# Optimization experiments

Hardware: AMD Instinct MI355X
Metric: run time of the kernel (lower is better)

Reference implementation:

```python
import jax, jax.numpy as jnp
import numpy as np

N_NODES = 100000
N_EDGES = 1600000
IN_FEATS = 128
HEADS = 4
OUT_FEATS = 32
NEG_SLOPE = 0.2


def setup_inputs() -> dict:
    key = jax.random.key(0)
    ks = jax.random.split(key, 7)
    x = jax.random.normal(ks[0], (N_NODES, IN_FEATS), dtype=jnp.float32)
    fc_w = jax.random.normal(ks[1], (HEADS * OUT_FEATS, IN_FEATS), dtype=jnp.float32) * (1.0 / np.sqrt(IN_FEATS))
    attn_l = jax.random.normal(ks[2], (HEADS, OUT_FEATS), dtype=jnp.float32) * (1.0 / np.sqrt(OUT_FEATS))
    attn_r = jax.random.normal(ks[3], (HEADS, OUT_FEATS), dtype=jnp.float32) * (1.0 / np.sqrt(OUT_FEATS))
    bias = jnp.zeros((HEADS * OUT_FEATS,), dtype=jnp.float32)
    src = jax.random.randint(ks[4], (N_EDGES,), 0, N_NODES, dtype=jnp.int64 if jax.config.jax_enable_x64 else jnp.int32)
    dst = jax.random.randint(ks[5], (N_EDGES,), 0, N_NODES, dtype=jnp.int64 if jax.config.jax_enable_x64 else jnp.int32)
    return {"x": x, "fc_w": fc_w, "attn_l": attn_l, "attn_r": attn_r, "bias": bias, "src": src, "dst": dst}


def reference(x, fc_w, attn_l, attn_r, bias, src, dst):
    """DGL GATConv (feat_drop=attn_drop=0, residual identity since in==H*D,
    allow_zero_in_degree=True, activation=None), then concat heads."""
    N = x.shape[0]
    H, D = attn_l.shape
    # linear projection: [N, H, D]
    feat = (x @ fc_w.T).reshape(N, H, D)
    # per-node attention halves: [N, H]
    el = jnp.einsum('nhd,hd->nh', feat, attn_l)
    er = jnp.einsum('nhd,hd->nh', feat, attn_r)
    # per-edge score with leaky relu: [E, H]
    e = el[src] + er[dst]
    e = jnp.where(e > 0, e, NEG_SLOPE * e)
    # edge softmax grouped by destination node
    emax = jax.ops.segment_max(e, dst, num_segments=N)          # [N, H]
    ee = jnp.exp(e - emax[dst])                                  # [E, H]
    denom = jax.ops.segment_sum(ee, dst, num_segments=N)        # [N, H]
    a = ee / jnp.maximum(denom[dst], jnp.float32(1e-38))         # [E, H]
    # weighted message + scatter aggregate: [N, H, D]
    msg = feat[src] * a[:, :, None]
    rst = jax.ops.segment_sum(msg, dst, num_segments=N)
    # residual (identity since in_feats == H*D) + bias
    rst = rst + x.reshape(N, H, D) + bias.reshape(1, H, D)
    # concat heads
    return rst.reshape(N, H * D)
```

## Files before the change

### kernel.cpp

```cpp
#include <hip/hip_runtime.h>
#include <math.h>

#define NEG_SLOPE 0.2f
#define PB 256
#define BKT_SHIFT 8

typedef __attribute__((ext_vector_type(8))) short bf16x8;
typedef __attribute__((ext_vector_type(4))) float f32x4;

__device__ __forceinline__ unsigned bf16_rne(float f) {
  unsigned u = __float_as_uint(f);
  return (u + 0x7fff + ((u >> 16) & 1)) >> 16;
}

__device__ __forceinline__ float lrelu_exp(float v) {
  v = v > 0.f ? v : NEG_SLOPE * v;
  return __expf(v);
}

__device__ __forceinline__ void local_blk_scan(const int* __restrict__ blk_sums,
                                               int* s_blk_off, int nb, int t) {
  if (t < 64) {
    const int v = (t < nb) ? blk_sums[t] : 0;
    int incl = v;
#pragma unroll
    for (int d = 1; d < 64; d <<= 1) {
      const int o = __shfl_up(incl, d);
      if (t >= d) incl += o;
    }
    s_blk_off[t] = incl - v;
  }
}

__global__ __launch_bounds__(256) void gemm_hist(
    const float* __restrict__ x, const float* __restrict__ fc_w,
    const float* __restrict__ attn_l, const float* __restrict__ attn_r,
    const int* __restrict__ dst, unsigned* __restrict__ featb,
    float* __restrict__ el, float* __restrict__ er, int* __restrict__ hist,
    int N, int E, int NB, int chunk, int G)
{
  __shared__ __align__(16) unsigned w_lds[128 * 68];
  __shared__ int h[512];
  const int t = threadIdx.x;

  if (blockIdx.x >= G) {
    const int k = blockIdx.x - G;
    for (int i = t; i < NB; i += 256) h[i] = 0;
    __syncthreads();
    const int beg = k * chunk, end = min(E, beg + chunk);
    for (int e = beg + t; e < end; e += 256)
      atomicAdd(&h[dst[e] >> BKT_SHIFT], 1);
    __syncthreads();
    for (int i = t; i < NB; i += 256) hist[i * PB + k] = h[i];
    return;
  }

  const int row_base = blockIdx.x * 64;
  {
    const int c = t >> 1, half = t & 1;
    const float* src = fc_w + (size_t)c * 128 + half * 64;
    unsigned* dstp = &w_lds[c * 68 + half * 32];
#pragma unroll
    for (int i = 0; i < 16; ++i) {
      const float4 v = *reinterpret_cast<const float4*>(src + i * 4);
      dstp[2 * i]     = bf16_rne(v.x) | (bf16_rne(v.y) << 16);
      dstp[2 * i + 1] = bf16_rne(v.z) | (bf16_rne(v.w) << 16);
    }
  }

  const int w = t >> 6;
  const int l = t & 63;
  const int cl = l & 15;
  const int g = l >> 4;

  const int arow = min(row_base + w * 16 + cl, N - 1);
  const float* __restrict__ xp = x + (size_t)arow * 128;
  bf16x8 a_frag[4];
#pragma unroll
  for (int ks = 0; ks < 4; ++ks) {
    const float4 v0 = *reinterpret_cast<const float4*>(xp + ks * 32 + g * 8);
    const float4 v1 =
        *reinterpret_cast<const float4*>(xp + ks * 32 + g * 8 + 4);
    uint4 uu;
    uu.x = bf16_rne(v0.x) | (bf16_rne(v0.y) << 16);
    uu.y = bf16_rne(v0.z) | (bf16_rne(v0.w) << 16);
    uu.z = bf16_rne(v1.x) | (bf16_rne(v1.y) << 16);
    uu.w = bf16_rne(v1.z) | (bf16_rne(v1.w) << 16);
    a_frag[ks] = *reinterpret_cast<bf16x8*>(&uu);
  }
  __syncthreads();

  f32x4 acc[8];
#pragma unroll
  for (int ct = 0; ct < 8; ++ct) acc[ct] = (f32x4){0.f, 0.f, 0.f, 0.f};

#pragma unroll
  for (int ct = 0; ct < 8; ++ct) {
#pragma unroll
    for (int ks = 0; ks < 4; ++ks) {
      const bf16x8 b_frag = *reinterpret_cast<const bf16x8*>(
          &w_lds[(ct * 16 + cl) * 68 + ks * 16 + g * 4]);
      acc[ct] = __builtin_amdgcn_mfma_f32_16x16x32_bf16(a_frag[ks], b_frag,
                                                        acc[ct], 0, 0, 0);
    }
  }

#pragma unroll
  for (int ct = 0; ct < 8; ++ct) {
#pragma unroll
    for (int r = 0; r < 4; ++r) {
      const float v = acc[ct][r];
      const float vn = __shfl_xor(v, 1);
      const int node = row_base + w * 16 + g * 4 + r;
      if ((cl & 1) == 0 && node < N) {
        featb[(size_t)node * 64 + ct * 8 + (cl >> 1)] =
            bf16_rne(v) | (bf16_rne(vn) << 16);
      }
    }
  }

  float al_lo[4], al_hi[4], ar_lo[4], ar_hi[4];
#pragma unroll
  for (int hh = 0; hh < 4; ++hh) {
    al_lo[hh] = attn_l[hh * 32 + cl];
    al_hi[hh] = attn_l[hh * 32 + 16 + cl];
    ar_lo[hh] = attn_r[hh * 32 + cl];
    ar_hi[hh] = attn_r[hh * 32 + 16 + cl];
  }
#pragma unroll
  for (int r = 0; r < 4; ++r) {
    const int node = row_base + w * 16 + g * 4 + r;
#pragma unroll
    for (int hh = 0; hh < 4; ++hh) {
      float pl = acc[2 * hh][r] * al_lo[hh] + acc[2 * hh + 1][r] * al_hi[hh];
      float pr = acc[2 * hh][r] * ar_lo[hh] + acc[2 * hh + 1][r] * ar_hi[hh];
#pragma unroll
      for (int d = 1; d < 16; d <<= 1) {
        pl += __shfl_xor(pl, d);
        pr += __shfl_xor(pr, d);
      }
      if (cl == 0 && node < N) {
        el[(size_t)node * 4 + hh] = pl;
        er[(size_t)node * 4 + hh] = pr;
      }
    }
  }
}

__global__ __launch_bounds__(256) void scan_a(const int* __restrict__ deg,
                                              int* __restrict__ offs,
                                              int* __restrict__ blk_sums,
                                              int n) {
  __shared__ int wsum[4];
  const int b = blockIdx.x, t = threadIdx.x;
  const int base = b * 2048 + t * 8;
  int v[8];
  int s = 0;
#pragma unroll
  for (int j = 0; j < 8; ++j) {
    v[j] = s;
    const int d = (base + j < n) ? deg[base + j] : 0;
    s += d;
  }
  const int lane = t & 63;
  int incl = s;
#pragma unroll
  for (int d = 1; d < 64; d <<= 1) {
    const int o = __shfl_up(incl, d);
    if (lane >= d) incl += o;
  }
  const int w = t >> 6;
  if (lane == 63) wsum[w] = incl;
  __syncthreads();
  int woff = 0;
  for (int ww = 0; ww < w; ++ww) woff += wsum[ww];
  const int thr_excl = woff + incl - s;
#pragma unroll
  for (int j = 0; j < 8; ++j)
    if (base + j < n) offs[base + j] = thr_excl + v[j];
  if (t == 255) blk_sums[b] = woff + incl;
}

__global__ __launch_bounds__(256) void part_scatter(
    const int* __restrict__ src, const int* __restrict__ dst,
    const int* __restrict__ hscan, const int* __restrict__ blk_sums,
    unsigned* __restrict__ part, int E, int NB, int chunk, int nb) {
  __shared__ int cur[512];
  __shared__ int s_blk_off[64];
  const int k = blockIdx.x, t = threadIdx.x;
  local_blk_scan(blk_sums, s_blk_off, nb, t);
  __syncthreads();
  for (int i = t; i < NB; i += 256) {
    const int m = i * PB + k;
    cur[i] = hscan[m] + s_blk_off[m >> 11];
  }
  __syncthreads();
  const int beg = k * chunk, end = min(E, beg + chunk);
  for (int e = beg + t; e < end; e += 256) {
    const int d = dst[e];
    const int b = d >> BKT_SHIFT;
    const int pos = atomicAdd(&cur[b], 1);
    part[pos] = (unsigned)src[e] |
                ((unsigned)(d & ((1 << BKT_SHIFT) - 1)) << 20);
  }
}

__global__ __launch_bounds__(512) void build_csr(
    const unsigned* __restrict__ part, const int* __restrict__ hscan,
    const int* __restrict__ blk_sums, const float* __restrict__ el,
    const float* __restrict__ er, int* __restrict__ node_offs,
    unsigned* __restrict__ csr, uint2* __restrict__ wsb,
    int N, int E, int NB, int nb) {
  __shared__ int cnt[256];
  __shared__ int wtot[4];
  __shared__ int s_blk_off[64];
  const int b = blockIdx.x, t = threadIdx.x;
  local_blk_scan(blk_sums, s_blk_off, nb, t);
  if (t < 256) cnt[t] = 0;
  __syncthreads();
  const int m0 = b * PB;
  const int bbase = hscan[m0] + s_blk_off[m0 >> 11];
  int bend = E;
  if (b + 1 < NB) {
    const int m1 = (b + 1) * PB;
    bend = hscan[m1] + s_blk_off[m1 >> 11];
  }
  const int node0 = b << BKT_SHIFT;
  for (int p = bbase + t; p < bend; p += 512)
    atomicAdd(&cnt[part[p] >> 20], 1);
  __syncthreads();
  int a0 = 0, incl = 0;
  if (t < 256) {
    a0 = cnt[t];
    incl = a0;
#pragma unroll
    for (int d1 = 1; d1 < 64; d1 <<= 1) {
      const int o = __shfl_up(incl, d1);
      if ((t & 63) >= d1) incl += o;
    }
    if ((t & 63) == 63) wtot[t >> 6] = incl;
  }
  __syncthreads();
  if (t < 256) {
    const int w = t >> 6;
    int woff = 0;
    for (int ww = 0; ww < w; ++ww) woff += wtot[ww];
    const int e0 = woff + incl - a0;
    cnt[t] = e0;
    if (node0 + t < N) node_offs[node0 + t] = bbase + e0;
    if (b == NB - 1 && t == 0) node_offs[N] = E;
  }
  __syncthreads();
  for (int p = bbase + t; p < bend; p += 512) {
    const unsigned v = part[p];
    const int lpos = atomicAdd(&cnt[v >> 20], 1);
    csr[bbase + lpos] = v;
  }
  __syncthreads();
  for (int p = bbase + t; p < bend; p += 512) {
    const unsigned v = csr[p];
    const unsigned s = v & 0xFFFFFu;
    const unsigned ld = v >> 20;
    const float4 l4 = *reinterpret_cast<const float4*>(el + s * 4);
    const float4 r4 =
        *reinterpret_cast<const float4*>(er + (unsigned)(node0 + ld) * 4);
    uint2 u;
    u.x = bf16_rne(lrelu_exp(l4.x + r4.x)) |
          (bf16_rne(lrelu_exp(l4.y + r4.y)) << 16);
    u.y = bf16_rne(lrelu_exp(l4.z + r4.z)) |
          (bf16_rne(lrelu_exp(l4.w + r4.w)) << 16);
    wsb[p] = u;
  }
}

__global__ __launch_bounds__(256) void agg_kernel(
    const uint4* __restrict__ featb4, const unsigned* __restrict__ csr,
    const unsigned short* __restrict__ wsb_us, const float* __restrict__ x,
    const float* __restrict__ bias, const int* __restrict__ node_offs,
    float* __restrict__ out, int N, int E)
{
  const int n = (int)((blockIdx.x * (size_t)blockDim.x + threadIdx.x) >> 6);
  if (n >= N) return;
  const unsigned lane = threadIdx.x & 63;
  const unsigned q = lane >> 4;
  const unsigned li = lane & 15;
  const unsigned hh = li >> 2;
  const unsigned short* __restrict__ wp = wsb_us + hh;
  const int beg = node_offs[n];
  const int end = node_offs[n + 1];
  const int nfull = (end - beg) >> 4;

  float a0 = 0.f, a1 = 0.f, a2 = 0.f, a3 = 0.f;
  float a4 = 0.f, a5 = 0.f, a6 = 0.f, a7 = 0.f, ds = 0.f;
  int p = beg;
  for (int gi = 0; gi < nfull; ++gi, p += 16) {
    unsigned pk[4]; unsigned wu[4]; uint4 fv[4];
#pragma unroll
    for (int i = 0; i < 4; ++i) pk[i] = csr[(unsigned)p + 4 * i + q];
#pragma unroll
    for (int i = 0; i < 4; ++i)
      wu[i] = wp[((unsigned)p + 4 * i + q) * 4];
#pragma unroll
    for (int i = 0; i < 4; ++i)
      fv[i] = featb4[(pk[i] & 0xFFFFFu) * 16 + li];
#pragma unroll
    for (int i = 0; i < 4; ++i) {
      const float w = __uint_as_float(wu[i] << 16);
      a0 = fmaf(w, __uint_as_float(fv[i].x << 16), a0);
      a1 = fmaf(w, __uint_as_float(fv[i].x & 0xffff0000u), a1);
      a2 = fmaf(w, __uint_as_float(fv[i].y << 16), a2);
      a3 = fmaf(w, __uint_as_float(fv[i].y & 0xffff0000u), a3);
      a4 = fmaf(w, __uint_as_float(fv[i].z << 16), a4);
      a5 = fmaf(w, __uint_as_float(fv[i].z & 0xffff0000u), a5);
      a6 = fmaf(w, __uint_as_float(fv[i].w << 16), a6);
      a7 = fmaf(w, __uint_as_float(fv[i].w & 0xffff0000u), a7);
      ds += w;
    }
  }
  if (p < end) {
    const int last = end - 1;
    unsigned pk[4]; unsigned wu[4]; uint4 fv[4]; int ee[4];
#pragma unroll
    for (int i = 0; i < 4; ++i) ee[i] = p + 4 * i + (int)q;
#pragma unroll
    for (int i = 0; i < 4; ++i) pk[i] = csr[(unsigned)min(ee[i], last)];
#pragma unroll
    for (int i = 0; i < 4; ++i)
      wu[i] = wp[(unsigned)min(ee[i], last) * 4];
#pragma unroll
    for (int i = 0; i < 4; ++i)
      fv[i] = featb4[(pk[i] & 0xFFFFFu) * 16 + li];
#pragma unroll
    for (int i = 0; i < 4; ++i) {
      float w = __uint_as_float(wu[i] << 16);
      if (ee[i] > last) w = 0.f;
      a0 = fmaf(w, __uint_as_float(fv[i].x << 16), a0);
      a1 = fmaf(w, __uint_as_float(fv[i].x & 0xffff0000u), a1);
      a2 = fmaf(w, __uint_as_float(fv[i].y << 16), a2);
      a3 = fmaf(w, __uint_as_float(fv[i].y & 0xffff0000u), a3);
      a4 = fmaf(w, __uint_as_float(fv[i].z << 16), a4);
      a5 = fmaf(w, __uint_as_float(fv[i].z & 0xffff0000u), a5);
      a6 = fmaf(w, __uint_as_float(fv[i].w << 16), a6);
      a7 = fmaf(w, __uint_as_float(fv[i].w & 0xffff0000u), a7);
      ds += w;
    }
  }

  a0 += __shfl_xor(a0, 16); a0 += __shfl_xor(a0, 32);
  a1 += __shfl_xor(a1, 16); a1 += __shfl_xor(a1, 32);
  a2 += __shfl_xor(a2, 16); a2 += __shfl_xor(a2, 32);
  a3 += __shfl_xor(a3, 16); a3 += __shfl_xor(a3, 32);
  a4 += __shfl_xor(a4, 16); a4 += __shfl_xor(a4, 32);
  a5 += __shfl_xor(a5, 16); a5 += __shfl_xor(a5, 32);
  a6 += __shfl_xor(a6, 16); a6 += __shfl_xor(a6, 32);
  a7 += __shfl_xor(a7, 16); a7 += __shfl_xor(a7, 32);
  ds += __shfl_xor(ds, 16); ds += __shfl_xor(ds, 32);

  if (q == 0) {
    const float inv = 1.f / fmaxf(ds, 1e-38f);
    const float4 x0 = ((const float4*)x)[(unsigned)n * 32 + 2 * li];
    const float4 x1 = ((const float4*)x)[(unsigned)n * 32 + 2 * li + 1];
    const float4 b0 = ((const float4*)bias)[2 * li];
    const float4 b1 = ((const float4*)bias)[2 * li + 1];
    float4 o0, o1;
    o0.x = fmaf(a0, inv, x0.x + b0.x);
    o0.y = fmaf(a1, inv, x0.y + b0.y);
    o0.z = fmaf(a2, inv, x0.z + b0.z);
    o0.w = fmaf(a3, inv, x0.w + b0.w);
    o1.x = fmaf(a4, inv, x1.x + b1.x);
    o1.y = fmaf(a5, inv, x1.y + b1.y);
    o1.z = fmaf(a6, inv, x1.z + b1.z);
    o1.w = fmaf(a7, inv, x1.w + b1.w);
    ((float4*)out)[(unsigned)n * 32 + 2 * li] = o0;
    ((float4*)out)[(unsigned)n * 32 + 2 * li + 1] = o1;
  }
}

extern "C" void kernel_launch(void* const* d_in, const int* in_sizes, int n_in,
                              void* d_out, int out_size, void* d_ws,
                              size_t ws_size, hipStream_t stream) {
  const float* x      = (const float*)d_in[0];
  const float* fc_w   = (const float*)d_in[1];
  const float* attn_l = (const float*)d_in[2];
  const float* attn_r = (const float*)d_in[3];
  const float* bias   = (const float*)d_in[4];
  const int*   src    = (const int*)d_in[5];
  const int*   dst    = (const int*)d_in[6];
  const int N = in_sizes[0] / 128;
  const int E = in_sizes[5];
  float* out = (float*)d_out;

  const int NB = (N + 255) >> 8;
  const int M = NB * PB;
  const int chunk = (E + PB - 1) / PB;
  const int nb = (M + 2047) / 2048;

  char* ws = (char*)d_ws;
  size_t off = 0;
  auto alloc = [&](size_t bytes) {
    void* p = ws + off;
    off += (bytes + 255) & ~(size_t)255;
    return p;
  };
  unsigned* featb   = (unsigned*)alloc((size_t)N * 128 * 2);
  float* el         = (float*)alloc((size_t)N * 4 * 4);
  float* er         = (float*)alloc((size_t)N * 4 * 4);
  int*   hist       = (int*)alloc((size_t)M * 4);
  int*   hscan      = (int*)alloc((size_t)(M + 1) * 4);
  int*   node_offs  = (int*)alloc((size_t)(N + 1) * 4);
  int*   blk_sums   = (int*)alloc(256);
  unsigned* part    = (unsigned*)alloc((size_t)E * 4);
  unsigned* csr     = (unsigned*)alloc((size_t)E * 4);
  uint2* wsb        = (uint2*)alloc((size_t)E * 8);

  const int G = (N + 63) / 64;
  gemm_hist<<<G + PB, 256, 0, stream>>>(x, fc_w, attn_l, attn_r, dst, featb,
                                        el, er, hist, N, E, NB, chunk, G);
  scan_a<<<nb, 256, 0, stream>>>(hist, hscan, blk_sums, M);
  part_scatter<<<PB, 256, 0, stream>>>(src, dst, hscan, blk_sums, part, E,
                                       NB, chunk, nb);
  build_csr<<<NB, 512, 0, stream>>>(part, hscan, blk_sums, el, er, node_offs,
                                    csr, wsb, N, E, NB, nb);
  agg_kernel<<<(N + 3) / 4, 256, 0, stream>>>((const uint4*)featb, csr,
                                              (const unsigned short*)wsb, x,
                                              bias, node_offs, out, N, E);
}
```

Before: 152.8 us.

## Shrink destination buckets to 64 nodes and widen scan chunk

New measurement: 170.1 us. 1.11x slower.

```diff
diff --git a/kernel.cpp b/kernel.cpp
--- a/kernel.cpp
+++ b/kernel.cpp
@@ -3,7 +3,8 @@
 
 #define NEG_SLOPE 0.2f
 #define PB 256
-#define BKT_SHIFT 8
+#define BKT_SHIFT 6
+#define SCAN_CHUNK 8192
 
 typedef __attribute__((ext_vector_type(8))) short bf16x8;
 typedef __attribute__((ext_vector_type(4))) float f32x4;
@@ -40,7 +41,7 @@
     int N, int E, int NB, int chunk, int G)
 {
   __shared__ __align__(16) unsigned w_lds[128 * 68];
-  __shared__ int h[512];
+  __shared__ int h[1600];
   const int t = threadIdx.x;
 
   if (blockIdx.x >= G) {
@@ -147,21 +148,16 @@
   }
 }
 
-__global__ __launch_bounds__(256) void scan_a(const int* __restrict__ deg,
-                                              int* __restrict__ offs,
+__global__ __launch_bounds__(256) void scan_a(const int* __restrict__ hist,
+                                              int* __restrict__ hscan,
                                               int* __restrict__ blk_sums,
                                               int n) {
   __shared__ int wsum[4];
   const int b = blockIdx.x, t = threadIdx.x;
-  const int base = b * 2048 + t * 8;
-  int v[8];
+  const int base = b * SCAN_CHUNK + t * 32;
   int s = 0;
 #pragma unroll
-  for (int j = 0; j < 8; ++j) {
-    v[j] = s;
-    const int d = (base + j < n) ? deg[base + j] : 0;
-    s += d;
-  }
+  for (int j = 0; j < 32; ++j) s += (base + j < n) ? hist[base + j] : 0;
   const int lane = t & 63;
   int incl = s;
 #pragma unroll
@@ -174,10 +170,14 @@
   __syncthreads();
   int woff = 0;
   for (int ww = 0; ww < w; ++ww) woff += wsum[ww];
-  const int thr_excl = woff + incl - s;
-#pragma unroll
-  for (int j = 0; j < 8; ++j)
-    if (base + j < n) offs[base + j] = thr_excl + v[j];
+  int run = woff + incl - s;
+#pragma unroll
+  for (int j = 0; j < 32; ++j) {
+    if (base + j < n) {
+      hscan[base + j] = run;
+      run += hist[base + j];
+    }
+  }
   if (t == 255) blk_sums[b] = woff + incl;
 }
 
@@ -185,14 +185,14 @@
     const int* __restrict__ src, const int* __restrict__ dst,
     const int* __restrict__ hscan, const int* __restrict__ blk_sums,
     unsigned* __restrict__ part, int E, int NB, int chunk, int nb) {
-  __shared__ int cur[512];
+  __shared__ int cur[1600];
   __shared__ int s_blk_off[64];
   const int k = blockIdx.x, t = threadIdx.x;
   local_blk_scan(blk_sums, s_blk_off, nb, t);
   __syncthreads();
   for (int i = t; i < NB; i += 256) {
     const int m = i * PB + k;
-    cur[i] = hscan[m] + s_blk_off[m >> 11];
+    cur[i] = hscan[m] + s_blk_off[m >> 13];
   }
   __syncthreads();
   const int beg = k * chunk, end = min(E, beg + chunk);
@@ -205,59 +205,50 @@
   }
 }
 
-__global__ __launch_bounds__(512) void build_csr(
+__global__ __launch_bounds__(256) void build_csr(
     const unsigned* __restrict__ part, const int* __restrict__ hscan,
     const int* __restrict__ blk_sums, const float* __restrict__ el,
     const float* __restrict__ er, int* __restrict__ node_offs,
     unsigned* __restrict__ csr, uint2* __restrict__ wsb,
     int N, int E, int NB, int nb) {
-  __shared__ int cnt[256];
-  __shared__ int wtot[4];
+  __shared__ int cnt[64];
   __shared__ int s_blk_off[64];
   const int b = blockIdx.x, t = threadIdx.x;
   local_blk_scan(blk_sums, s_blk_off, nb, t);
-  if (t < 256) cnt[t] = 0;
+  if (t < 64) cnt[t] = 0;
   __syncthreads();
   const int m0 = b * PB;
-  const int bbase = hscan[m0] + s_blk_off[m0 >> 11];
+  const int bbase = hscan[m0] + s_blk_off[m0 >> 13];
   int bend = E;
   if (b + 1 < NB) {
     const int m1 = (b + 1) * PB;
-    bend = hscan[m1] + s_blk_off[m1 >> 11];
+    bend = hscan[m1] + s_blk_off[m1 >> 13];
   }
   const int node0 = b << BKT_SHIFT;
-  for (int p = bbase + t; p < bend; p += 512)
+  for (int p = bbase + t; p < bend; p += 256)
     atomicAdd(&cnt[part[p] >> 20], 1);
   __syncthreads();
-  int a0 = 0, incl = 0;
-  if (t < 256) {
-    a0 = cnt[t];
-    incl = a0;
+  if (t < 64) {
+    const int a0 = cnt[t];
+    int incl = a0;
 #pragma unroll
     for (int d1 = 1; d1 < 64; d1 <<= 1) {
       const int o = __shfl_up(incl, d1);
-      if ((t & 63) >= d1) incl += o;
-    }
-    if ((t & 63) == 63) wtot[t >> 6] = incl;
-  }
-  __syncthreads();
-  if (t < 256) {
-    const int w = t >> 6;
-    int woff = 0;
-    for (int ww = 0; ww < w; ++ww) woff += wtot[ww];
-    const int e0 = woff + incl - a0;
+      if (t >= d1) incl += o;
+    }
+    const int e0 = incl - a0;
     cnt[t] = e0;
     if (node0 + t < N) node_offs[node0 + t] = bbase + e0;
     if (b == NB - 1 && t == 0) node_offs[N] = E;
   }
   __syncthreads();
-  for (int p = bbase + t; p < bend; p += 512) {
+  for (int p = bbase + t; p < bend; p += 256) {
     const unsigned v = part[p];
     const int lpos = atomicAdd(&cnt[v >> 20], 1);
     csr[bbase + lpos] = v;
   }
   __syncthreads();
-  for (int p = bbase + t; p < bend; p += 512) {
+  for (int p = bbase + t; p < bend; p += 256) {
     const unsigned v = csr[p];
     const unsigned s = v & 0xFFFFFu;
     const unsigned ld = v >> 20;
@@ -390,10 +381,10 @@
   const int E = in_sizes[5];
   float* out = (float*)d_out;
 
-  const int NB = (N + 255) >> 8;
+  const int NB = (N + 63) >> 6;
   const int M = NB * PB;
   const int chunk = (E + PB - 1) / PB;
-  const int nb = (M + 2047) / 2048;
+  const int nb = (M + SCAN_CHUNK - 1) / SCAN_CHUNK;
 
   char* ws = (char*)d_ws;
   size_t off = 0;
@@ -419,7 +410,7 @@
   scan_a<<<nb, 256, 0, stream>>>(hist, hscan, blk_sums, M);
   part_scatter<<<PB, 256, 0, stream>>>(src, dst, hscan, blk_sums, part, E,
                                        NB, chunk, nb);
-  build_csr<<<NB, 512, 0, stream>>>(part, hscan, blk_sums, el, er, node_offs,
+  build_csr<<<NB, 256, 0, stream>>>(part, hscan, blk_sums, el, er, node_offs,
                                     csr, wsb, N, E, NB, nb);
   agg_kernel<<<(N + 3) / 4, 256, 0, stream>>>((const uint4*)featb, csr,
                                               (const unsigned short*)wsb, x,
```
